# Performance work log

Measured on AMD Instinct MI355X. Metric: run time of the kernel, lower is better.

Reference implementation:

```python
import jax, jax.numpy as jnp
import numpy as np

K = 499  # kernel_size


def setup_inputs() -> dict:
    key = jax.random.key(0)
    k1, k2 = jax.random.split(key)
    B, F, T = 32, 64, 8000
    # nonnegative spectrogram input, shape (B, 1, F, T)
    x = jax.random.uniform(k1, (B, 1, F, T), dtype=jnp.float32)
    a = 0.90 + 0.099 * jax.random.uniform(k2, (F,), dtype=jnp.float32)
    w = jnp.ones((F,), dtype=jnp.float32)
    return {"x": x, "a": a, "w": w}


def _build_kernel(a, w, dtype):
    # powers[f, k] = a_f ** k, k = 0..K-2
    F = a.shape[0]
    powers = a[:, None] ** jnp.arange(K - 1, dtype=dtype)  # (F, K-1)
    C = 1.0 / powers.sum(axis=1)                            # (F,)
    neg = (-C * w)[:, None] * powers                        # (F, K-1)
    # pre-flip kernel = [1, neg_0, ..., neg_{K-2}]; flipped -> [neg_{K-2}, ..., neg_0, 1]
    kern = jnp.concatenate([neg[:, ::-1], jnp.ones((F, 1), dtype)], axis=1)  # (F, K)
    return kern[:, None, :]  # (F, 1, K) OIH, groups = F


def reference(x, a, w):
    dtype = x.dtype
    kern = _build_kernel(a.astype(dtype), w.astype(dtype), dtype)
    xs = x[:, 0]  # (B, F, T)
    # replicate (edge) pad on the left by K-1 along time
    xp = jnp.pad(xs, ((0, 0), (0, 0), (K - 1, 0)), mode="edge")
    y = jax.lax.conv_general_dilated(
        xp, kern,
        window_strides=(1,), padding="VALID",
        dimension_numbers=("NCH", "OIH", "NCH"),
        feature_group_count=xs.shape[1],
    )  # (B, F, T)
    return jnp.abs(y)[:, None]  # (B, 1, F, T)
```

## Files before the change

### kernel.cpp

```cpp
#include <hip/hip_runtime.h>
#include <math.h>


constexpr int T     = 8000;
constexpr int F     = 64;
constexpr int B     = 32;
constexpr int KM1   = 498;
constexpr int NSEG  = 4;
constexpr int SEGLEN = T / NSEG;
constexpr int ROUND = 256;
constexpr int NFULL = SEGLEN / ROUND;
constexpr int TAILN = SEGLEN - NFULL * ROUND;

__global__ __launch_bounds__(256) void willmore_scan_kernel(
    const float* __restrict__ x, const float* __restrict__ a,
    const float* __restrict__ w, float* __restrict__ out)
{
    const int row  = blockIdx.x;
    const int seg  = threadIdx.x >> 6;
    const int lane = threadIdx.x & 63;
    const int f = row % F;

    const float* xr   = x   + (size_t)row * T;
    float*       orow = out + (size_t)row * T;

    const double ad = (double)a[f];
    double p = ad, a498d = 1.0;
    for (int e = KM1; e; e >>= 1) { if (e & 1) a498d *= p; p *= p; }
    const double sumgeo = (1.0 - a498d) / (1.0 - ad);
    const float  af     = (float)ad;
    const float  na498  = (float)(-a498d);
    const float  g      = (float)(1.0 / sumgeo) * w[f];
    const double a4d    = ad * ad * ad * ad;
    const float  alane  = (float)exp2(log2(a4d) * (double)lane);
    float wstep[6];
    double tpow = a4d;
    #pragma unroll
    for (int s = 0; s < 6; ++s) { wstep[s] = (float)tpow; tpow *= tpow; }
    const float a256 = (float)tpow;

    const int t0 = seg * SEGLEN;

    float S;
    {
        const int base = t0 - 512 + 8 * lane;
        float xs[8];
        if (t0 == 0) {
            #pragma unroll
            for (int i = 0; i < 8; ++i) xs[i] = xr[max(base + i, 0)];
        } else {
            const float4 v0 = *(const float4*)(xr + base);
            const float4 v1 = *(const float4*)(xr + base + 4);
            xs[0]=v0.x; xs[1]=v0.y; xs[2]=v0.z; xs[3]=v0.w;
            xs[4]=v1.x; xs[5]=v1.y; xs[6]=v1.z; xs[7]=v1.w;
        }
        #pragma unroll
        for (int i = 0; i < 8; ++i) { if (511 - 8*lane - i >= KM1) xs[i] = 0.0f; }
        float h = xs[0];
        #pragma unroll
        for (int i = 1; i < 8; ++i) h = fmaf(h, af, xs[i]);
        const int e = 504 - 8 * lane;
        float wl = 1.0f, pb = af;
        #pragma unroll
        for (int s = 0; s < 9; ++s) { if (e & (1 << s)) wl *= pb; pb *= pb; }
        float contrib = wl * h;
        #pragma unroll
        for (int s = 1; s < 64; s <<= 1) contrib += __shfl_xor(contrib, s, 64);
        S = contrib;
    }

    int tR = t0;
    for (int rnd = 0; rnd <= NFULL; ++rnd, tR += ROUND) {
        const bool tail = (rnd == NFULL);
        const int tbase = tR + 4 * lane;

        float4 xv;
        if (!tail) {
            xv = *(const float4*)(xr + tbase);
        } else {
            xv.x = xr[min(tbase,     T - 1)];
            xv.y = xr[min(tbase + 1, T - 1)];
            xv.z = xr[min(tbase + 2, T - 1)];
            xv.w = xr[min(tbase + 3, T - 1)];
        }

        const int lag = tbase - KM1;
        float l0, l1, l2, l3;
        if (lag >= 0 && !tail) {
            const float2* lp = (const float2*)(xr + lag);
            const float2 la = lp[0], lb = lp[1];
            l0 = la.x; l1 = la.y; l2 = lb.x; l3 = lb.y;
        } else {
            l0 = xr[max(min(lag,     T - 1), 0)];
            l1 = xr[max(min(lag + 1, T - 1), 0)];
            l2 = xr[max(min(lag + 2, T - 1), 0)];
            l3 = xr[max(min(lag + 3, T - 1), 0)];
        }

        const float u0 = fmaf(na498, l0, xv.x);
        const float u1 = fmaf(na498, l1, xv.y);
        const float u2 = fmaf(na498, l2, xv.z);
        const float u3 = fmaf(na498, l3, xv.w);

        const float q1 = fmaf(af, u0, u1);
        const float q2 = fmaf(af, q1, u2);
        const float q3 = fmaf(af, q2, u3);

        float G = q3;
        #pragma unroll
        for (int s = 0; s < 6; ++s) {
            const float gup = __shfl_up(G, 1 << s, 64);
            const float ws  = (lane >= (1 << s)) ? wstep[s] : 0.0f;
            G = fmaf(ws, gup, G);
        }
        float Gprev = __shfl_up(G, 1, 64);
        if (lane == 0) Gprev = 0.0f;

        const float s0 = fmaf(alane, S, Gprev);
        const float y0 = fabsf(fmaf(-g, s0, xv.x));
        const float s1 = fmaf(af, s0, u0);
        const float y1 = fabsf(fmaf(-g, s1, xv.y));
        const float s2 = fmaf(af, s1, u1);
        const float y2 = fabsf(fmaf(-g, s2, xv.z));
        const float s3 = fmaf(af, s2, u2);
        const float y3 = fabsf(fmaf(-g, s3, xv.w));

        if (!tail) {
            *(float4*)(orow + tbase) = make_float4(y0, y1, y2, y3);
            const float Slast = __shfl(G, 63, 64);
            S = fmaf(a256, S, Slast);
        } else if (4 * lane < TAILN) {
            *(float4*)(orow + tbase) = make_float4(y0, y1, y2, y3);
        }
    }
}

extern "C" void kernel_launch(void* const* d_in, const int* in_sizes, int n_in,
                              void* d_out, int out_size, void* d_ws, size_t ws_size,
                              hipStream_t stream) {
    const float* x = (const float*)d_in[0];
    const float* a = (const float*)d_in[1];
    const float* w = (const float*)d_in[2];
    float* out = (float*)d_out;

    const int blocks = B * F;
    hipLaunchKernelGGL(willmore_scan_kernel, dim3(blocks), dim3(256), 0, stream,
                       x, a, w, out);
}
```

Baseline: 122.5 us.

## Process 8 samples per lane and use DPP wave scan for recurrence

Each lane now handles 8 consecutive samples, so a 64-lane round covers 512 samples and there are fewer rounds. The cross-lane prefix scan of the linear recurrence uses DPP row shifts and row broadcasts instead of __shfl_up, and the per-lane exclusive value is recovered by subtracting and dividing by a^8 rather than by an extra shuffle. Lane-invariant powers are computed in double by a helper, and the carry uses readlane. This aims to cut shuffle and LDS-permute latency and per-sample loop overhead, at the cost of more registers per lane and possible precision loss from the division by r.

```diff
diff --git a/kernel.cpp b/kernel.cpp
--- a/kernel.cpp
+++ b/kernel.cpp
@@ -2,15 +2,24 @@
 #include <math.h>
 
 
-constexpr int T     = 8000;
-constexpr int F     = 64;
-constexpr int B     = 32;
-constexpr int KM1   = 498;
-constexpr int NSEG  = 4;
+constexpr int T      = 8000;
+constexpr int F      = 64;
+constexpr int B      = 32;
+constexpr int KM1    = 498;
+constexpr int NSEG   = 4;
 constexpr int SEGLEN = T / NSEG;
-constexpr int ROUND = 256;
-constexpr int NFULL = SEGLEN / ROUND;
-constexpr int TAILN = SEGLEN - NFULL * ROUND;
+constexpr int ROUND  = 512;
+constexpr int NFULL  = SEGLEN / ROUND;
+constexpr int TAILN  = SEGLEN - NFULL * ROUND;
+
+#define DPP_F(x, ctrl, rm) \
+  __builtin_bit_cast(float, __builtin_amdgcn_update_dpp(0, __builtin_bit_cast(int, (x)), (ctrl), (rm), 0xf, false))
+
+__device__ __forceinline__ double dpow(double b, int e) {
+    double r = 1.0, p = b;
+    while (e) { if (e & 1) r *= p; p *= p; e >>= 1; }
+    return r;
+}
 
 __global__ __launch_bounds__(256) void willmore_scan_kernel(
     const float* __restrict__ x, const float* __restrict__ a,
@@ -24,113 +33,104 @@
     const float* xr   = x   + (size_t)row * T;
     float*       orow = out + (size_t)row * T;
 
-    const double ad = (double)a[f];
-    double p = ad, a498d = 1.0;
-    for (int e = KM1; e; e >>= 1) { if (e & 1) a498d *= p; p *= p; }
+    const double ad     = (double)a[f];
+    const double a498d  = dpow(ad, KM1);
     const double sumgeo = (1.0 - a498d) / (1.0 - ad);
+    const double r_d    = dpow(ad, 8);
     const float  af     = (float)ad;
     const float  na498  = (float)(-a498d);
     const float  g      = (float)(1.0 / sumgeo) * w[f];
-    const double a4d    = ad * ad * ad * ad;
-    const float  alane  = (float)exp2(log2(a4d) * (double)lane);
-    float wstep[6];
-    double tpow = a4d;
-    #pragma unroll
-    for (int s = 0; s < 6; ++s) { wstep[s] = (float)tpow; tpow *= tpow; }
-    const float a256 = (float)tpow;
+    const float  r1     = (float)r_d;
+    const float  r2     = (float)(r_d * r_d);
+    const float  r4     = (float)dpow(r_d, 4);
+    const float  r8     = (float)dpow(r_d, 8);
+    const float  a512   = (float)dpow(r_d, 64);
+    const float  inv_r  = (float)(1.0 / r_d);
+    const float  alane  = (float)dpow(r_d, lane);
+    const float  wA     = (float)dpow(r_d, (lane & 15) + 1);
+    const float  wB     = (float)dpow(r_d, (lane & 31) + 1);
 
     const int t0 = seg * SEGLEN;
 
     float S;
-    {
+    if (t0 == 0) {
+        S = xr[0] * (float)sumgeo;
+    } else {
         const int base = t0 - 512 + 8 * lane;
-        float xs[8];
-        if (t0 == 0) {
-            #pragma unroll
-            for (int i = 0; i < 8; ++i) xs[i] = xr[max(base + i, 0)];
-        } else {
-            const float4 v0 = *(const float4*)(xr + base);
-            const float4 v1 = *(const float4*)(xr + base + 4);
-            xs[0]=v0.x; xs[1]=v0.y; xs[2]=v0.z; xs[3]=v0.w;
-            xs[4]=v1.x; xs[5]=v1.y; xs[6]=v1.z; xs[7]=v1.w;
-        }
+        const float4 v0 = *(const float4*)(xr + base);
+        const float4 v1 = *(const float4*)(xr + base + 4);
+        float xs[8] = {v0.x, v0.y, v0.z, v0.w, v1.x, v1.y, v1.z, v1.w};
         #pragma unroll
-        for (int i = 0; i < 8; ++i) { if (511 - 8*lane - i >= KM1) xs[i] = 0.0f; }
+        for (int i = 0; i < 8; ++i) { if (511 - 8 * lane - i >= KM1) xs[i] = 0.0f; }
         float h = xs[0];
         #pragma unroll
         for (int i = 1; i < 8; ++i) h = fmaf(h, af, xs[i]);
-        const int e = 504 - 8 * lane;
-        float wl = 1.0f, pb = af;
-        #pragma unroll
-        for (int s = 0; s < 9; ++s) { if (e & (1 << s)) wl *= pb; pb *= pb; }
-        float contrib = wl * h;
+        float contrib = (float)dpow(ad, 504 - 8 * lane) * h;
         #pragma unroll
         for (int s = 1; s < 64; s <<= 1) contrib += __shfl_xor(contrib, s, 64);
         S = contrib;
     }
 
-    int tR = t0;
-    for (int rnd = 0; rnd <= NFULL; ++rnd, tR += ROUND) {
-        const bool tail = (rnd == NFULL);
-        const int tbase = tR + 4 * lane;
+    #pragma unroll
+    for (int rnd = 0; rnd <= NFULL; ++rnd) {
+        const bool last = (rnd == NFULL);
+        const int tR = t0 + rnd * ROUND;
+        int tb = tR + 8 * lane;
+        if (last) tb = min(tb, T - 8);
 
-        float4 xv;
-        if (!tail) {
-            xv = *(const float4*)(xr + tbase);
+        const float4 v0 = *(const float4*)(xr + tb);
+        const float4 v1 = *(const float4*)(xr + tb + 4);
+        const float xv[8] = {v0.x, v0.y, v0.z, v0.w, v1.x, v1.y, v1.z, v1.w};
+
+        const int lg = tb - KM1;
+        float lv[8];
+        if (t0 == 0 && rnd == 0) {
+            #pragma unroll
+            for (int i = 0; i < 8; ++i) lv[i] = xr[max(lg + i, 0)];
         } else {
-            xv.x = xr[min(tbase,     T - 1)];
-            xv.y = xr[min(tbase + 1, T - 1)];
-            xv.z = xr[min(tbase + 2, T - 1)];
-            xv.w = xr[min(tbase + 3, T - 1)];
+            const float2 p0 = *(const float2*)(xr + lg);
+            const float2 p1 = *(const float2*)(xr + lg + 2);
+            const float2 p2 = *(const float2*)(xr + lg + 4);
+            const float2 p3 = *(const float2*)(xr + lg + 6);
+            lv[0]=p0.x; lv[1]=p0.y; lv[2]=p1.x; lv[3]=p1.y;
+            lv[4]=p2.x; lv[5]=p2.y; lv[6]=p3.x; lv[7]=p3.y;
         }
 
-        const int lag = tbase - KM1;
-        float l0, l1, l2, l3;
-        if (lag >= 0 && !tail) {
-            const float2* lp = (const float2*)(xr + lag);
-            const float2 la = lp[0], lb = lp[1];
-            l0 = la.x; l1 = la.y; l2 = lb.x; l3 = lb.y;
-        } else {
-            l0 = xr[max(min(lag,     T - 1), 0)];
-            l1 = xr[max(min(lag + 1, T - 1), 0)];
-            l2 = xr[max(min(lag + 2, T - 1), 0)];
-            l3 = xr[max(min(lag + 3, T - 1), 0)];
+        float u[8];
+        #pragma unroll
+        for (int i = 0; i < 8; ++i) u[i] = fmaf(na498, lv[i], xv[i]);
+
+        float q = u[0];
+        #pragma unroll
+        for (int i = 1; i < 8; ++i) q = fmaf(q, af, u[i]);
+
+        float G = q;
+        G = fmaf(r1, DPP_F(G, 0x111, 0xf), G);
+        G = fmaf(r2, DPP_F(G, 0x112, 0xf), G);
+        G = fmaf(r4, DPP_F(G, 0x114, 0xf), G);
+        G = fmaf(r8, DPP_F(G, 0x118, 0xf), G);
+        G = fmaf(wA, DPP_F(G, 0x142, 0xa), G);
+        G = fmaf(wB, DPP_F(G, 0x143, 0xc), G);
+
+        const float E = (G - q) * inv_r;
+
+        float s = fmaf(alane, S, E);
+        float y[8];
+        #pragma unroll
+        for (int i = 0; i < 8; ++i) {
+            y[i] = fabsf(fmaf(-g, s, xv[i]));
+            s = fmaf(af, s, u[i]);
         }
 
-        const float u0 = fmaf(na498, l0, xv.x);
-        const float u1 = fmaf(na498, l1, xv.y);
-        const float u2 = fmaf(na498, l2, xv.z);
-        const float u3 = fmaf(na498, l3, xv.w);
+        if (!last || lane < TAILN / 8) {
+            *(float4*)(orow + tb)     = make_float4(y[0], y[1], y[2], y[3]);
+            *(float4*)(orow + tb + 4) = make_float4(y[4], y[5], y[6], y[7]);
+        }
 
-        const float q1 = fmaf(af, u0, u1);
-        const float q2 = fmaf(af, q1, u2);
-        const float q3 = fmaf(af, q2, u3);
-
-        float G = q3;
-        #pragma unroll
-        for (int s = 0; s < 6; ++s) {
-            const float gup = __shfl_up(G, 1 << s, 64);
-            const float ws  = (lane >= (1 << s)) ? wstep[s] : 0.0f;
-            G = fmaf(ws, gup, G);
-        }
-        float Gprev = __shfl_up(G, 1, 64);
-        if (lane == 0) Gprev = 0.0f;
-
-        const float s0 = fmaf(alane, S, Gprev);
-        const float y0 = fabsf(fmaf(-g, s0, xv.x));
-        const float s1 = fmaf(af, s0, u0);
-        const float y1 = fabsf(fmaf(-g, s1, xv.y));
-        const float s2 = fmaf(af, s1, u1);
-        const float y2 = fabsf(fmaf(-g, s2, xv.z));
-        const float s3 = fmaf(af, s2, u2);
-        const float y3 = fabsf(fmaf(-g, s3, xv.w));
-
-        if (!tail) {
-            *(float4*)(orow + tbase) = make_float4(y0, y1, y2, y3);
-            const float Slast = __shfl(G, 63, 64);
-            S = fmaf(a256, S, Slast);
-        } else if (4 * lane < TAILN) {
-            *(float4*)(orow + tbase) = make_float4(y0, y1, y2, y3);
+        if (!last) {
+            const float G63 = __builtin_bit_cast(float,
+                __builtin_amdgcn_readlane(__builtin_bit_cast(int, G), 63));
+            S = fmaf(a512, S, G63);
         }
     }
 }
```

Measured after the change: 123.6 us. About the same (+0.9%).
